# Optimization experiments

Hardware: AMD Instinct MI355X
Metric: run time of the kernel (lower is better)

Reference implementation:

```python
import jax, jax.numpy as jnp
import numpy as np

N = 10000      # nodes
E = 160000     # edges
K = 32         # MC samples (dim 1 of inputs)
D_IN = 128
D_OUT = 32


def setup_inputs() -> dict:
    key = jax.random.key(0)
    k1, k2, k3, k4, k5 = jax.random.split(key, 5)
    x = jax.random.normal(k1, (N, K, D_IN), dtype=jnp.float32)
    # Glorot-uniform weight as in weight_variable_glorot
    init_range = np.sqrt(6.0 / (D_IN + D_OUT))
    weights = jax.random.uniform(k2, (D_IN, D_OUT), dtype=jnp.float32,
                                 minval=-init_range, maxval=init_range)
    edge_row = jax.random.randint(k3, (E,), 0, N, dtype=jnp.int32)
    edge_col = jax.random.randint(k4, (E,), 0, N, dtype=jnp.int32)
    edge_val = jax.random.uniform(k5, (E,), dtype=jnp.float32)
    return {"x": x, "weights": weights, "edge_row": edge_row,
            "edge_col": edge_col, "edge_val": edge_val}


def reference(x, weights, edge_row, edge_col, edge_val):
    # Original loops over K slices doing: dropout(p=0) -> x @ W -> spmm(adj, x) -> relu,
    # then concatenates along axis 1. Batched equivalent:
    h = jnp.einsum('nkd,de->nke', x, weights)            # [N, K, D_OUT]
    # sparse adj @ h : out[r] += val * h[c] for each edge (r, c, val)
    msg = h[edge_col] * edge_val[:, None, None]          # [E, K, D_OUT]
    agg = jax.ops.segment_sum(msg, edge_row, num_segments=N)  # [N, K, D_OUT]
    return jax.nn.relu(agg)
```

## Files before the change

kernel.cpp:

```cpp
#include <hip/hip_runtime.h>
#include <hip/hip_bf16.h>

#define KK 32
#define DIN 128
#define DOUT 32
#define NVEC (KK * DOUT)
#define MBKT 64
#define OCAP 4096

typedef float        vf4    __attribute__((ext_vector_type(4)));
typedef unsigned int vu4    __attribute__((ext_vector_type(4)));
typedef short        bf16x8 __attribute__((ext_vector_type(8)));

__device__ __forceinline__ float bfu2f(unsigned int u) {
    return __uint_as_float(u << 16);
}
__device__ __forceinline__ unsigned int f2bfu(float f) {
    __hip_bfloat16 b = __float2bfloat16(f);
    return *(unsigned short*)&b;
}

__global__ __launch_bounds__(256) void prep_kernel(
    int* __restrict__ p, int n,
    const float* __restrict__ w, unsigned short* __restrict__ wfrag)
{
    int i = blockIdx.x * 256 + threadIdx.x;
    if (i < n) p[i] = 0;
    if (blockIdx.x == 0) {
        for (int item = threadIdx.x; item < 512; item += 256) {
            int lane = item & 63;
            int fk   = item >> 6;
            int nt   = fk >> 2, ks = fk & 3;
            int q    = lane >> 4, lm = lane & 15;
            #pragma unroll
            for (int j = 0; j < 8; ++j) {
                int k = ks * 32 + q * 8 + j;
                wfrag[(size_t)item * 8 + j] =
                    (unsigned short)f2bfu(w[k * DOUT + nt * 16 + lm]);
            }
        }
    }
}

__global__ __launch_bounds__(256) void gemm_fill_kernel(
    const float* __restrict__ x, const unsigned short* __restrict__ wfrag,
    unsigned short* __restrict__ h,
    const int* __restrict__ erow, const int* __restrict__ ecol,
    const float* __restrict__ eval, int* __restrict__ cursor,
    uint2* __restrict__ bedge,
    int* __restrict__ ocnt, int* __restrict__ orow,
    int* __restrict__ ocol, float* __restrict__ oval,
    int E, int FB)
{
    const int tid = threadIdx.x;

    if (blockIdx.x < (unsigned)FB) {
        int i = blockIdx.x * 256 + tid;
        if (i >= E) return;
        int r = __builtin_nontemporal_load(erow + i);
        int p = atomicAdd(&cursor[r], 1);
        if (p < MBKT) {
            uint2 e;
            e.x = (unsigned int)__builtin_nontemporal_load(ecol + i);
            e.y = __float_as_uint(__builtin_nontemporal_load(eval + i));
            bedge[r * MBKT + p] = e;
        } else {
            int q = atomicAdd(ocnt, 1);
            if (q < OCAP) {
                orow[q] = r;
                ocol[q] = ecol[i];
                oval[q] = eval[i];
            }
        }
        return;
    }

    const int lane = tid & 63;
    const int wid  = tid >> 6;
    const int q    = lane >> 4;
    const int lm   = lane & 15;

    bf16x8 bf[2][4];
    {
        const bf16x8* wf = (const bf16x8*)wfrag;
        #pragma unroll
        for (int nt = 0; nt < 2; ++nt)
            #pragma unroll
            for (int ks = 0; ks < 4; ++ks)
                bf[nt][ks] = wf[(nt * 4 + ks) * 64 + lane];
    }

    const int tile = (blockIdx.x - FB) * 4 + wid;
    const int r0   = tile * 16;
    const float* xrow = x + (size_t)(r0 + lm) * DIN + q * 8;

    vf4 acc0 = {0.f, 0.f, 0.f, 0.f};
    vf4 acc1 = {0.f, 0.f, 0.f, 0.f};

    #pragma unroll
    for (int ks = 0; ks < 4; ++ks) {
        vf4 a0 = __builtin_nontemporal_load((const vf4*)(xrow + ks * 32));
        vf4 a1 = __builtin_nontemporal_load((const vf4*)(xrow + ks * 32 + 4));
        bf16x8 af;
        af[0] = (short)f2bfu(a0.x); af[1] = (short)f2bfu(a0.y);
        af[2] = (short)f2bfu(a0.z); af[3] = (short)f2bfu(a0.w);
        af[4] = (short)f2bfu(a1.x); af[5] = (short)f2bfu(a1.y);
        af[6] = (short)f2bfu(a1.z); af[7] = (short)f2bfu(a1.w);
        acc0 = __builtin_amdgcn_mfma_f32_16x16x32_bf16(af, bf[0][ks], acc0, 0, 0, 0);
        acc1 = __builtin_amdgcn_mfma_f32_16x16x32_bf16(af, bf[1][ks], acc1, 0, 0, 0);
    }

    #pragma unroll
    for (int q2 = 0; q2 < 4; ++q2) {
        unsigned int pk = f2bfu(acc0[q2]) | (f2bfu(acc1[q2]) << 16);
        *(unsigned int*)(h + (size_t)(r0 + q * 4 + q2) * DOUT + lm * 2) = pk;
    }
}

__global__ __launch_bounds__(256) void agg_kernel(
    const unsigned short* __restrict__ h, const int* __restrict__ cursor,
    const uint2* __restrict__ bedge,
    const int* __restrict__ ocnt, const int* __restrict__ orow,
    const int* __restrict__ ocol, const float* __restrict__ oval,
    float* __restrict__ out)
{
    const int tid  = threadIdx.x;
    const int half = tid >> 7;
    const int lt   = tid & 127;
    const int lane = tid & 63;
    const int r    = blockIdx.x * 2 + half;

    const int deg  = cursor[r];
    const int degb = deg < MBKT ? deg : MBKT;
    const int on0  = *ocnt;

    int   ec = 0;
    float ev = 0.f;
    if (lane < degb) {
        uint2 e = bedge[r * MBKT + lane];
        ec = (int)e.x;
        ev = __uint_as_float(e.y);
    }

    float acc[8];
    #pragma unroll
    for (int q = 0; q < 8; ++q) acc[q] = 0.f;

    #pragma unroll 8
    for (int j = 0; j < degb; ++j) {
        int   c = __shfl(ec, j, 64);
        float v = __shfl(ev, j, 64);
        vu4 p = *(const vu4*)(h + (size_t)c * NVEC + lt * 8);
        acc[0] += v * bfu2f(p.x & 0xffffu);
        acc[1] += v * bfu2f(p.x >> 16);
        acc[2] += v * bfu2f(p.y & 0xffffu);
        acc[3] += v * bfu2f(p.y >> 16);
        acc[4] += v * bfu2f(p.z & 0xffffu);
        acc[5] += v * bfu2f(p.z >> 16);
        acc[6] += v * bfu2f(p.w & 0xffffu);
        acc[7] += v * bfu2f(p.w >> 16);
    }

    if (on0 > 0) {
        int on = on0 > OCAP ? OCAP : on0;
        for (int q = 0; q < on; ++q) {
            if (orow[q] == r) {
                int   c = ocol[q];
                float v = oval[q];
                vu4 p = *(const vu4*)(h + (size_t)c * NVEC + lt * 8);
                acc[0] += v * bfu2f(p.x & 0xffffu);
                acc[1] += v * bfu2f(p.x >> 16);
                acc[2] += v * bfu2f(p.y & 0xffffu);
                acc[3] += v * bfu2f(p.y >> 16);
                acc[4] += v * bfu2f(p.z & 0xffffu);
                acc[5] += v * bfu2f(p.z >> 16);
                acc[6] += v * bfu2f(p.w & 0xffffu);
                acc[7] += v * bfu2f(p.w >> 16);
            }
        }
    }

    vf4 oA, oB;
    oA.x = fmaxf(acc[0], 0.f); oA.y = fmaxf(acc[2], 0.f);
    oA.z = fmaxf(acc[4], 0.f); oA.w = fmaxf(acc[6], 0.f);
    oB.x = fmaxf(acc[1], 0.f); oB.y = fmaxf(acc[3], 0.f);
    oB.z = fmaxf(acc[5], 0.f); oB.w = fmaxf(acc[7], 0.f);
    float* obase = out + (size_t)r * NVEC + (lt >> 2) * 32 + (lt & 3) * 4;
    __builtin_nontemporal_store(oA, (vf4*)obase);
    __builtin_nontemporal_store(oB, (vf4*)(obase + 16));
}

extern "C" void kernel_launch(void* const* d_in, const int* in_sizes, int n_in,
                              void* d_out, int out_size, void* d_ws, size_t ws_size,
                              hipStream_t stream)
{
    const float* x    = (const float*)d_in[0];
    const float* w    = (const float*)d_in[1];
    const int*   erow = (const int*)d_in[2];
    const int*   ecol = (const int*)d_in[3];
    const float* eval = (const float*)d_in[4];
    float* out = (float*)d_out;

    const int E = in_sizes[2];
    const int N = in_sizes[0] / (KK * DIN);
    const int R = N * KK;

    char* ws = (char*)d_ws;
    size_t off = 0;
    auto take = [&](size_t bytes) {
        void* p = ws + off;
        off += (bytes + 15) & ~(size_t)15;
        return p;
    };
    unsigned short* h = (unsigned short*)take((size_t)R * DOUT * sizeof(unsigned short));
    int*   cursor = (int*)take((size_t)(N + 1) * sizeof(int));
    uint2* bedge  = (uint2*)take((size_t)N * MBKT * sizeof(uint2));
    int*   orow   = (int*)take((size_t)OCAP * sizeof(int));
    int*   ocol   = (int*)take((size_t)OCAP * sizeof(int));
    float* oval   = (float*)take((size_t)OCAP * sizeof(float));
    unsigned short* wfrag = (unsigned short*)take((size_t)512 * 8 * sizeof(unsigned short));
    int*   ocnt   = cursor + N;
    (void)ws_size;

    const int FB = (E + 255) / 256;
    const int GB = (R / 16) / 4;

    prep_kernel<<<(N + 1 + 255) / 256, 256, 0, stream>>>(cursor, N + 1, w, wfrag);
    gemm_fill_kernel<<<FB + GB, 256, 0, stream>>>(
        x, wfrag, h, erow, ecol, eval, cursor, bedge, ocnt, orow, ocol, oval, E, FB);
    agg_kernel<<<N / 2, 256, 0, stream>>>(
        h, cursor, bedge, ocnt, orow, ocol, oval, out);
}
```

Before: 298.2 us.

## Split aggregation per node across eight blocks with one wave each

```diff
diff --git a/kernel.cpp b/kernel.cpp
--- a/kernel.cpp
+++ b/kernel.cpp
@@ -10,6 +10,7 @@
 
 typedef float        vf4    __attribute__((ext_vector_type(4)));
 typedef unsigned int vu4    __attribute__((ext_vector_type(4)));
+typedef unsigned int vu2    __attribute__((ext_vector_type(2)));
 typedef short        bf16x8 __attribute__((ext_vector_type(8)));
 
 __device__ __forceinline__ float bfu2f(unsigned int u) {
@@ -122,43 +123,40 @@
     const uint2* __restrict__ bedge,
     const int* __restrict__ ocnt, const int* __restrict__ orow,
     const int* __restrict__ ocol, const float* __restrict__ oval,
-    float* __restrict__ out)
+    float* __restrict__ out, int N)
 {
     const int tid  = threadIdx.x;
-    const int half = tid >> 7;
-    const int lt   = tid & 127;
+    const int wid  = tid >> 6;
     const int lane = tid & 63;
-    const int r    = blockIdx.x * 2 + half;
-
-    const int deg  = cursor[r];
+    const int g    = blockIdx.x & 7;
+    const int r    = (blockIdx.x >> 3) * 4 + wid;
+    if (r >= N) return;
+
+    const int deg  = __builtin_nontemporal_load(cursor + r);
     const int degb = deg < MBKT ? deg : MBKT;
     const int on0  = *ocnt;
 
     int   ec = 0;
     float ev = 0.f;
     if (lane < degb) {
-        uint2 e = bedge[r * MBKT + lane];
+        vu2 e = __builtin_nontemporal_load(
+            (const vu2*)bedge + r * MBKT + lane);
         ec = (int)e.x;
         ev = __uint_as_float(e.y);
     }
 
-    float acc[8];
-    #pragma unroll
-    for (int q = 0; q < 8; ++q) acc[q] = 0.f;
+    const unsigned int* hb = (const unsigned int*)h;
+    const int loff = g * 64 + lane;
+
+    float a0 = 0.f, a1 = 0.f;
 
     #pragma unroll 8
     for (int j = 0; j < degb; ++j) {
         int   c = __shfl(ec, j, 64);
         float v = __shfl(ev, j, 64);
-        vu4 p = *(const vu4*)(h + (size_t)c * NVEC + lt * 8);
-        acc[0] += v * bfu2f(p.x & 0xffffu);
-        acc[1] += v * bfu2f(p.x >> 16);
-        acc[2] += v * bfu2f(p.y & 0xffffu);
-        acc[3] += v * bfu2f(p.y >> 16);
-        acc[4] += v * bfu2f(p.z & 0xffffu);
-        acc[5] += v * bfu2f(p.z >> 16);
-        acc[6] += v * bfu2f(p.w & 0xffffu);
-        acc[7] += v * bfu2f(p.w >> 16);
+        unsigned int p = hb[(size_t)c * 512 + loff];
+        a0 += v * bfu2f(p & 0xffffu);
+        a1 += v * bfu2f(p >> 16);
     }
 
     if (on0 > 0) {
@@ -167,27 +165,18 @@
             if (orow[q] == r) {
                 int   c = ocol[q];
                 float v = oval[q];
-                vu4 p = *(const vu4*)(h + (size_t)c * NVEC + lt * 8);
-                acc[0] += v * bfu2f(p.x & 0xffffu);
-                acc[1] += v * bfu2f(p.x >> 16);
-                acc[2] += v * bfu2f(p.y & 0xffffu);
-                acc[3] += v * bfu2f(p.y >> 16);
-                acc[4] += v * bfu2f(p.z & 0xffffu);
-                acc[5] += v * bfu2f(p.z >> 16);
-                acc[6] += v * bfu2f(p.w & 0xffffu);
-                acc[7] += v * bfu2f(p.w >> 16);
+                unsigned int p = hb[(size_t)c * 512 + loff];
+                a0 += v * bfu2f(p & 0xffffu);
+                a1 += v * bfu2f(p >> 16);
             }
         }
     }
 
-    vf4 oA, oB;
-    oA.x = fmaxf(acc[0], 0.f); oA.y = fmaxf(acc[2], 0.f);
-    oA.z = fmaxf(acc[4], 0.f); oA.w = fmaxf(acc[6], 0.f);
-    oB.x = fmaxf(acc[1], 0.f); oB.y = fmaxf(acc[3], 0.f);
-    oB.z = fmaxf(acc[5], 0.f); oB.w = fmaxf(acc[7], 0.f);
-    float* obase = out + (size_t)r * NVEC + (lt >> 2) * 32 + (lt & 3) * 4;
-    __builtin_nontemporal_store(oA, (vf4*)obase);
-    __builtin_nontemporal_store(oB, (vf4*)(obase + 16));
+    float o0 = fmaxf(a0, 0.f);
+    float o1 = fmaxf(a1, 0.f);
+    float* ob = out + (size_t)r * NVEC + (4 * g + (lane >> 4)) * 32 + (lane & 15);
+    __builtin_nontemporal_store(o0, ob);
+    __builtin_nontemporal_store(o1, ob + 16);
 }
 
 extern "C" void kernel_launch(void* const* d_in, const int* in_sizes, int n_in,
@@ -228,6 +217,6 @@
     prep_kernel<<<(N + 1 + 255) / 256, 256, 0, stream>>>(cursor, N + 1, w, wfrag);
     gemm_fill_kernel<<<FB + GB, 256, 0, stream>>>(
         x, wfrag, h, erow, ecol, eval, cursor, bedge, ocnt, orow, ocol, oval, E, FB);
-    agg_kernel<<<N / 2, 256, 0, stream>>>(
-        h, cursor, bedge, ocnt, orow, ocol, oval, out);
-}
+    agg_kernel<<<((N + 3) / 4) * 8, 256, 0, stream>>>(
+        h, cursor, bedge, ocnt, orow, ocol, oval, out, N);
+}
```

Measured after the change: 326.3 us. 9.4% more time.
